# Performance work log

Hardware: AMD Instinct MI355X
Metric: run time of the kernel (lower is better)

## Reference

```python
import jax, jax.numpy as jnp
import numpy as np

B, N, E, D = 4, 50000, 800000, 64


def setup_inputs() -> dict:
    key = jax.random.key(0)
    k_h, k_e, k_w1, k_w2 = jax.random.split(key, 4)
    s = 1.0 / np.sqrt(D)  # glorot-ish scale for 64x64 linear weights
    return {
        "t": jnp.zeros((1,), jnp.float32),
        "h": jax.random.normal(k_h, (B, N, D), jnp.float32),
        "edge_index": jax.random.randint(k_e, (2, E), 0, N, jnp.int32),
        "W1": jax.random.normal(k_w1, (D, D), jnp.float32) * s,
        "b1": jnp.zeros((D,), jnp.float32),
        "W2": jax.random.normal(k_w2, (D, D), jnp.float32) * s,
        "b2": jnp.zeros((D,), jnp.float32),
    }


def _gcn(x, row, col, norm, W, b, n_nodes):
    # x: (B, N, D). PyG GCNConv: linear (no bias) -> normalized gather/scatter -> +bias
    xw = jnp.einsum("bnd,de->bne", x, W)
    msg = xw[:, row, :] * norm[None, :, None]          # (B, E+N, D)
    agg = jax.vmap(lambda m: jax.ops.segment_sum(m, col, num_segments=n_nodes))(msg)
    return agg + b


def reference(t, h, edge_index, W1, b1, W2, b2):
    n_nodes = h.shape[1]
    loop = jnp.arange(n_nodes, dtype=edge_index.dtype)
    # add self-loops (PyG GCNConv default)
    row = jnp.concatenate([edge_index[0], loop])  # source nodes
    col = jnp.concatenate([edge_index[1], loop])  # target nodes
    # symmetric normalization D^{-1/2} (A+I) D^{-1/2}; degree counted on targets
    deg = jax.ops.segment_sum(jnp.ones_like(row, dtype=h.dtype), col, num_segments=n_nodes)
    dis = jnp.where(deg > 0, jax.lax.rsqrt(deg), 0.0)
    norm = dis[row] * dis[col]
    h = jnp.tanh(_gcn(h, row, col, norm, W1, b1, n_nodes))
    h = jnp.tanh(_gcn(h, row, col, norm, W2, b2, n_nodes))
    return h
```

## Files before the change

### kernel.cpp

```cpp
#include <hip/hip_runtime.h>
#include <math.h>

#define B_ 4
#define N_ 50000
#define E_ 800000
#define D_ 64
#define M_ (B_*N_)
#define STRIDE_ 48

#define FILL_BLKS_ ((E_/4+255)/256)

typedef _Float16 h4 __attribute__((ext_vector_type(4)));
typedef _Float16 h8 __attribute__((ext_vector_type(8)));
typedef float    f4 __attribute__((ext_vector_type(4)));

__device__ __forceinline__ void wfrag_one(const float* __restrict__ W, h8* __restrict__ Wf, int fid) {
  int khalf = fid >> 8, rem = fid & 255, tt = rem >> 6, lane = rem & 63;
  int kq = lane >> 4, m = lane & 15;
  h8 v;
#pragma unroll
  for (int j = 0; j < 8; j++) {
    int k = khalf * 32 + kq * 8 + j;
    v[j] = (_Float16)W[k * 64 + tt * 16 + m];
  }
  Wf[fid] = v;
}

__global__ __launch_bounds__(256) void k_fill(const int4* __restrict__ row4, const int4* __restrict__ col4,
                                              int* __restrict__ cur, int* __restrict__ em,
                                              const float* __restrict__ W1, const float* __restrict__ W2,
                                              h8* __restrict__ Wf1, h8* __restrict__ Wf2) {
  if (blockIdx.x >= FILL_BLKS_) {
    int fa = (blockIdx.x - FILL_BLKS_) * 256 + threadIdx.x;
    if (fa < 512) wfrag_one(W1, Wf1, fa);
    else          wfrag_one(W2, Wf2, fa - 512);
    return;
  }
  int e = blockIdx.x * 256 + threadIdx.x;
  if (e < E_ / 4) {
    int4 c = col4[e];
    int4 r = row4[e];
    int k;
    k = atomicAdd(&cur[c.x], 1); if (k < STRIDE_) em[c.x * STRIDE_ + k] = r.x << 9;
    k = atomicAdd(&cur[c.y], 1); if (k < STRIDE_) em[c.y * STRIDE_ + k] = r.y << 9;
    k = atomicAdd(&cur[c.z], 1); if (k < STRIDE_) em[c.z * STRIDE_ + k] = r.z << 9;
    k = atomicAdd(&cur[c.w], 1); if (k < STRIDE_) em[c.w * STRIDE_ + k] = r.w << 9;
  }
}

template<int IN_F16>
__global__ __launch_bounds__(256) void k_linear(const void* __restrict__ Xv,
                                                const h8* __restrict__ Wf,
                                                const int* __restrict__ cur,
                                                _Float16* __restrict__ Y) {
  int wv = blockIdx.x * 4 + (threadIdx.x >> 6);
  int lane = threadIdx.x & 63;
  int m = lane & 15, kq = lane >> 4;
  size_t r0 = (size_t)wv * 16;
  h8 a0, a1;
  if constexpr (IN_F16) {
    const _Float16* xr = (const _Float16*)Xv + (r0 + m) * 64 + kq * 8;
    a0 = *(const h8*)(xr);
    a1 = *(const h8*)(xr + 32);
  } else {
    const float* xr = (const float*)Xv + (r0 + m) * 64 + kq * 8;
    f4 f0 = *(const f4*)(xr);
    f4 f1 = *(const f4*)(xr + 4);
    f4 f2 = *(const f4*)(xr + 32);
    f4 f3 = *(const f4*)(xr + 36);
#pragma unroll
    for (int j = 0; j < 4; j++) {
      a0[j] = (_Float16)f0[j]; a0[j + 4] = (_Float16)f1[j];
      a1[j] = (_Float16)f2[j]; a1[j + 4] = (_Float16)f3[j];
    }
  }
  f4 acc[4];
#pragma unroll
  for (int t = 0; t < 4; t++) {
    h8 b0 = Wf[t * 64 + lane];
    h8 b1 = Wf[256 + t * 64 + lane];
    f4 c = {0.f, 0.f, 0.f, 0.f};
    c = __builtin_amdgcn_mfma_f32_16x16x32_f16(a0, b0, c, 0, 0, 0);
    c = __builtin_amdgcn_mfma_f32_16x16x32_f16(a1, b1, c, 0, 0, 0);
    acc[t] = c;
  }
  int b  = (int)(r0 / N_);
  int n0 = (int)(r0 - (size_t)b * N_);
  float dv[4];
#pragma unroll
  for (int rr = 0; rr < 4; rr++) {
    int dg = cur[n0 + kq * 4 + rr];
    dv[rr] = 1.0f / sqrtf((float)(dg + 1));
  }
#pragma unroll
  for (int t = 0; t < 4; t++) {
#pragma unroll
    for (int rr = 0; rr < 4; rr++) {
      int n = n0 + kq * 4 + rr;
      Y[(size_t)n * 256 + b * 64 + t * 16 + m] = (_Float16)(acc[t][rr] * dv[rr]);
    }
  }
}

template<int OUT_F16>
__global__ __launch_bounds__(512) void k_agg(const _Float16* __restrict__ xw,
                                             const int* __restrict__ cur,
                                             const int* __restrict__ em,
                                             const float* __restrict__ bias,
                                             void* __restrict__ outv) {
  int node = blockIdx.x * 8 + (threadIdx.x >> 6);
  int lane = threadIdx.x & 63;
  const char* xb = (const char*)xw + (size_t)(lane * 8);
  int deg = __builtin_amdgcn_readfirstlane(cur[node]);
  if (deg > STRIDE_) deg = STRIDE_;
  float dc = 1.0f / sqrtf((float)(deg + 1));
  h4 sv = *(const h4*)(xb + ((size_t)node << 9));
  f4 acc = __builtin_convertvector(sv, f4);
  const int* eb = em + node * STRIDE_;
#define EDGE_(o) do { \
    h4 v_ = *(const h4*)(xb + (unsigned)(o)); \
    acc += __builtin_convertvector(v_, f4); \
  } while (0)
  int j = 0;
  for (; j + 8 <= deg; j += 8) {
    int o0 = eb[j],     o1 = eb[j + 1], o2 = eb[j + 2], o3 = eb[j + 3];
    int o4 = eb[j + 4], o5 = eb[j + 5], o6 = eb[j + 6], o7 = eb[j + 7];
    EDGE_(o0); EDGE_(o1); EDGE_(o2); EDGE_(o3);
    EDGE_(o4); EDGE_(o5); EDGE_(o6); EDGE_(o7);
  }
  for (; j < deg; ++j) { int o = eb[j]; EDGE_(o); }
#undef EDGE_
  int b  = lane >> 4;
  int d0 = (lane & 15) * 4;
  f4 bb = *(const f4*)(bias + d0);
  float r0 = tanhf(acc.x * dc + bb.x);
  float r1 = tanhf(acc.y * dc + bb.y);
  float r2 = tanhf(acc.z * dc + bb.z);
  float r3 = tanhf(acc.w * dc + bb.w);
  if constexpr (OUT_F16) {
    h4 o;
    o[0] = (_Float16)r0; o[1] = (_Float16)r1;
    o[2] = (_Float16)r2; o[3] = (_Float16)r3;
    *(h4*)((_Float16*)outv + ((size_t)b * N_ + node) * 64 + d0) = o;
  } else {
    f4 r = {r0, r1, r2, r3};
    *(f4*)((float*)outv + ((size_t)b * N_ + node) * 64 + d0) = r;
  }
}

extern "C" void kernel_launch(void* const* d_in, const int* in_sizes, int n_in,
                              void* d_out, int out_size, void* d_ws, size_t ws_size,
                              hipStream_t stream) {
  const float* h  = (const float*)d_in[1];
  const int*   ei = (const int*)d_in[2];
  const float* W1 = (const float*)d_in[3];
  const float* b1 = (const float*)d_in[4];
  const float* W2 = (const float*)d_in[5];
  const float* b2 = (const float*)d_in[6];
  float* out = (float*)d_out;
  const int* row = ei;
  const int* col = ei + E_;

  char* p = (char*)d_ws;
  _Float16* xw = (_Float16*)p; p += (size_t)M_ * D_ * sizeof(_Float16);
  int*  em  = (int*)p;    p += (size_t)N_ * STRIDE_ * sizeof(int);
  int*  cur = (int*)p;    p += (size_t)N_ * sizeof(int);
  h8*   Wf1 = (h8*)p;     p += 512 * sizeof(h8);
  h8*   Wf2 = (h8*)p;     p += 512 * sizeof(h8);
  _Float16* h1 = (_Float16*)d_out;

  hipMemsetAsync(cur, 0, N_ * sizeof(int), stream);

  k_fill<<<FILL_BLKS_ + 4, 256, 0, stream>>>((const int4*)row, (const int4*)col, cur, em, W1, W2, Wf1, Wf2);
  k_linear<0><<<M_ / 64, 256, 0, stream>>>(h, Wf1, cur, xw);
  k_agg<1><<<N_ / 8, 512, 0, stream>>>(xw, cur, em, b1, h1);
  k_linear<1><<<M_ / 64, 256, 0, stream>>>(h1, Wf2, cur, xw);
  k_agg<0><<<N_ / 8, 512, 0, stream>>>(xw, cur, em, b2, out);
}
```

Baseline: 298.3 us.

## Fuse second linear layer into first aggregation and pack edge indices to 16-bit

Performs the second layer's 64x64 linear transform inside the first aggregation kernel. It stages each node's tanh outputs in shared memory and runs MFMA, which removes one kernel launch and the intermediate write/read of the hidden activations. Edge source indices are stored as 16-bit values instead of pre-shifted 32-bit offsets, halving index storage and read traffic. The fused MFMA uses only 4 of 16 rows, wasting matrix throughput and adding a block barrier. The 16-bit indices rely on N fitting in 16 bits.

```diff
diff --git a/kernel.cpp b/kernel.cpp
--- a/kernel.cpp
+++ b/kernel.cpp
@@ -13,6 +13,8 @@
 typedef _Float16 h4 __attribute__((ext_vector_type(4)));
 typedef _Float16 h8 __attribute__((ext_vector_type(8)));
 typedef float    f4 __attribute__((ext_vector_type(4)));
+typedef unsigned short ushort_t;
+typedef unsigned int  uint_t;
 
 __device__ __forceinline__ void wfrag_one(const float* __restrict__ W, h8* __restrict__ Wf, int fid) {
   int khalf = fid >> 8, rem = fid & 255, tt = rem >> 6, lane = rem & 63;
@@ -27,7 +29,7 @@
 }
 
 __global__ __launch_bounds__(256) void k_fill(const int4* __restrict__ row4, const int4* __restrict__ col4,
-                                              int* __restrict__ cur, int* __restrict__ em,
+                                              int* __restrict__ cur, ushort_t* __restrict__ em,
                                               const float* __restrict__ W1, const float* __restrict__ W2,
                                               h8* __restrict__ Wf1, h8* __restrict__ Wf2) {
   if (blockIdx.x >= FILL_BLKS_) {
@@ -41,38 +43,31 @@
     int4 c = col4[e];
     int4 r = row4[e];
     int k;
-    k = atomicAdd(&cur[c.x], 1); if (k < STRIDE_) em[c.x * STRIDE_ + k] = r.x << 9;
-    k = atomicAdd(&cur[c.y], 1); if (k < STRIDE_) em[c.y * STRIDE_ + k] = r.y << 9;
-    k = atomicAdd(&cur[c.z], 1); if (k < STRIDE_) em[c.z * STRIDE_ + k] = r.z << 9;
-    k = atomicAdd(&cur[c.w], 1); if (k < STRIDE_) em[c.w * STRIDE_ + k] = r.w << 9;
-  }
-}
-
-template<int IN_F16>
-__global__ __launch_bounds__(256) void k_linear(const void* __restrict__ Xv,
-                                                const h8* __restrict__ Wf,
-                                                const int* __restrict__ cur,
-                                                _Float16* __restrict__ Y) {
+    k = atomicAdd(&cur[c.x], 1); if (k < STRIDE_) em[c.x * STRIDE_ + k] = (ushort_t)r.x;
+    k = atomicAdd(&cur[c.y], 1); if (k < STRIDE_) em[c.y * STRIDE_ + k] = (ushort_t)r.y;
+    k = atomicAdd(&cur[c.z], 1); if (k < STRIDE_) em[c.z * STRIDE_ + k] = (ushort_t)r.z;
+    k = atomicAdd(&cur[c.w], 1); if (k < STRIDE_) em[c.w * STRIDE_ + k] = (ushort_t)r.w;
+  }
+}
+
+__global__ __launch_bounds__(256) void k_linear1(const float* __restrict__ X,
+                                                 const h8* __restrict__ Wf,
+                                                 const int* __restrict__ cur,
+                                                 _Float16* __restrict__ Y) {
   int wv = blockIdx.x * 4 + (threadIdx.x >> 6);
   int lane = threadIdx.x & 63;
   int m = lane & 15, kq = lane >> 4;
   size_t r0 = (size_t)wv * 16;
+  const float* xr = X + (r0 + m) * 64 + kq * 8;
+  f4 f0 = *(const f4*)(xr);
+  f4 f1 = *(const f4*)(xr + 4);
+  f4 f2 = *(const f4*)(xr + 32);
+  f4 f3 = *(const f4*)(xr + 36);
   h8 a0, a1;
-  if constexpr (IN_F16) {
-    const _Float16* xr = (const _Float16*)Xv + (r0 + m) * 64 + kq * 8;
-    a0 = *(const h8*)(xr);
-    a1 = *(const h8*)(xr + 32);
-  } else {
-    const float* xr = (const float*)Xv + (r0 + m) * 64 + kq * 8;
-    f4 f0 = *(const f4*)(xr);
-    f4 f1 = *(const f4*)(xr + 4);
-    f4 f2 = *(const f4*)(xr + 32);
-    f4 f3 = *(const f4*)(xr + 36);
-#pragma unroll
-    for (int j = 0; j < 4; j++) {
-      a0[j] = (_Float16)f0[j]; a0[j + 4] = (_Float16)f1[j];
-      a1[j] = (_Float16)f2[j]; a1[j + 4] = (_Float16)f3[j];
-    }
+#pragma unroll
+  for (int j = 0; j < 4; j++) {
+    a0[j] = (_Float16)f0[j]; a0[j + 4] = (_Float16)f1[j];
+    a1[j] = (_Float16)f2[j]; a1[j + 4] = (_Float16)f3[j];
   }
   f4 acc[4];
 #pragma unroll
@@ -102,50 +97,111 @@
   }
 }
 
-template<int OUT_F16>
-__global__ __launch_bounds__(512) void k_agg(const _Float16* __restrict__ xw,
-                                             const int* __restrict__ cur,
-                                             const int* __restrict__ em,
-                                             const float* __restrict__ bias,
-                                             void* __restrict__ outv) {
+#define AGG_GATHER_(xb, eb, deg, acc)                                            \
+  do {                                                                           \
+    int j_ = 0;                                                                  \
+    for (; j_ + 8 <= (deg); j_ += 8) {                                           \
+      uint_t u0 = (eb)[(j_ >> 1)],     u1 = (eb)[(j_ >> 1) + 1];                 \
+      uint_t u2 = (eb)[(j_ >> 1) + 2], u3 = (eb)[(j_ >> 1) + 3];                 \
+      h4 v0 = *(const h4*)((xb) + ((u0 & 0xFFFFu) << 9));                        \
+      h4 v1 = *(const h4*)((xb) + ((u0 >> 16) << 9));                            \
+      h4 v2 = *(const h4*)((xb) + ((u1 & 0xFFFFu) << 9));                        \
+      h4 v3 = *(const h4*)((xb) + ((u1 >> 16) << 9));                            \
+      h4 v4 = *(const h4*)((xb) + ((u2 & 0xFFFFu) << 9));                        \
+      h4 v5 = *(const h4*)((xb) + ((u2 >> 16) << 9));                            \
+      h4 v6 = *(const h4*)((xb) + ((u3 & 0xFFFFu) << 9));                        \
+      h4 v7 = *(const h4*)((xb) + ((u3 >> 16) << 9));                            \
+      acc += __builtin_convertvector(v0, f4);                                    \
+      acc += __builtin_convertvector(v1, f4);                                    \
+      acc += __builtin_convertvector(v2, f4);                                    \
+      acc += __builtin_convertvector(v3, f4);                                    \
+      acc += __builtin_convertvector(v4, f4);                                    \
+      acc += __builtin_convertvector(v5, f4);                                    \
+      acc += __builtin_convertvector(v6, f4);                                    \
+      acc += __builtin_convertvector(v7, f4);                                    \
+    }                                                                            \
+    for (; j_ < (deg); ++j_) {                                                   \
+      uint_t u_ = (eb)[j_ >> 1];                                                 \
+      uint_t o_ = ((j_ & 1) ? (u_ >> 16) : (u_ & 0xFFFFu)) << 9;                 \
+      h4 v_ = *(const h4*)((xb) + o_);                                           \
+      acc += __builtin_convertvector(v_, f4);                                    \
+    }                                                                            \
+  } while (0)
+
+__global__ __launch_bounds__(512) void k_agg1(const _Float16* __restrict__ xw,
+                                              const int* __restrict__ cur,
+                                              const ushort_t* __restrict__ em,
+                                              const float* __restrict__ bias,
+                                              const h8* __restrict__ Wf,
+                                              _Float16* __restrict__ Y) {
+  __shared__ _Float16 ys[8][256];
+  int w    = threadIdx.x >> 6;
+  int node = blockIdx.x * 8 + w;
+  int lane = threadIdx.x & 63;
+  const char* xb = (const char*)xw + (size_t)(lane * 8);
+  int degt = __builtin_amdgcn_readfirstlane(cur[node]);
+  int deg  = degt > STRIDE_ ? STRIDE_ : degt;
+  float dc = 1.0f / sqrtf((float)(degt + 1));
+  h4 sv = *(const h4*)(xb + ((size_t)node << 9));
+  f4 acc = __builtin_convertvector(sv, f4);
+  const uint_t* eb = (const uint_t*)(em + node * STRIDE_);
+  AGG_GATHER_(xb, eb, deg, acc);
+  int d0 = (lane & 15) * 4;
+  f4 bb = *(const f4*)(bias + d0);
+  h4 yv;
+  yv[0] = (_Float16)tanhf(acc.x * dc + bb.x);
+  yv[1] = (_Float16)tanhf(acc.y * dc + bb.y);
+  yv[2] = (_Float16)tanhf(acc.z * dc + bb.z);
+  yv[3] = (_Float16)tanhf(acc.w * dc + bb.w);
+  *(h4*)&ys[w][lane * 4] = yv;
+  __syncthreads();
+  int m = lane & 15, kq = lane >> 4;
+  h8 a0, a1;
+#pragma unroll
+  for (int q = 0; q < 8; q++) { a0[q] = (_Float16)0.f; a1[q] = (_Float16)0.f; }
+  if (m < 4) {
+    a0 = *(const h8*)&ys[w][m * 64 + kq * 8];
+    a1 = *(const h8*)&ys[w][m * 64 + 32 + kq * 8];
+  }
+#pragma unroll
+  for (int t = 0; t < 4; t++) {
+    h8 b0 = Wf[t * 64 + lane];
+    h8 b1 = Wf[256 + t * 64 + lane];
+    f4 c = {0.f, 0.f, 0.f, 0.f};
+    c = __builtin_amdgcn_mfma_f32_16x16x32_f16(a0, b0, c, 0, 0, 0);
+    c = __builtin_amdgcn_mfma_f32_16x16x32_f16(a1, b1, c, 0, 0, 0);
+    if (kq == 0) {
+#pragma unroll
+      for (int b2 = 0; b2 < 4; b2++)
+        Y[(size_t)node * 256 + b2 * 64 + t * 16 + m] = (_Float16)(c[b2] * dc);
+    }
+  }
+}
+
+__global__ __launch_bounds__(512) void k_agg2(const _Float16* __restrict__ xw,
+                                              const int* __restrict__ cur,
+                                              const ushort_t* __restrict__ em,
+                                              const float* __restrict__ bias,
+                                              float* __restrict__ out) {
   int node = blockIdx.x * 8 + (threadIdx.x >> 6);
   int lane = threadIdx.x & 63;
   const char* xb = (const char*)xw + (size_t)(lane * 8);
-  int deg = __builtin_amdgcn_readfirstlane(cur[node]);
-  if (deg > STRIDE_) deg = STRIDE_;
-  float dc = 1.0f / sqrtf((float)(deg + 1));
+  int degt = __builtin_amdgcn_readfirstlane(cur[node]);
+  int deg  = degt > STRIDE_ ? STRIDE_ : degt;
+  float dc = 1.0f / sqrtf((float)(degt + 1));
   h4 sv = *(const h4*)(xb + ((size_t)node << 9));
   f4 acc = __builtin_convertvector(sv, f4);
-  const int* eb = em + node * STRIDE_;
-#define EDGE_(o) do { \
-    h4 v_ = *(const h4*)(xb + (unsigned)(o)); \
-    acc += __builtin_convertvector(v_, f4); \
-  } while (0)
-  int j = 0;
-  for (; j + 8 <= deg; j += 8) {
-    int o0 = eb[j],     o1 = eb[j + 1], o2 = eb[j + 2], o3 = eb[j + 3];
-    int o4 = eb[j + 4], o5 = eb[j + 5], o6 = eb[j + 6], o7 = eb[j + 7];
-    EDGE_(o0); EDGE_(o1); EDGE_(o2); EDGE_(o3);
-    EDGE_(o4); EDGE_(o5); EDGE_(o6); EDGE_(o7);
-  }
-  for (; j < deg; ++j) { int o = eb[j]; EDGE_(o); }
-#undef EDGE_
+  const uint_t* eb = (const uint_t*)(em + node * STRIDE_);
+  AGG_GATHER_(xb, eb, deg, acc);
   int b  = lane >> 4;
   int d0 = (lane & 15) * 4;
   f4 bb = *(const f4*)(bias + d0);
-  float r0 = tanhf(acc.x * dc + bb.x);
-  float r1 = tanhf(acc.y * dc + bb.y);
-  float r2 = tanhf(acc.z * dc + bb.z);
-  float r3 = tanhf(acc.w * dc + bb.w);
-  if constexpr (OUT_F16) {
-    h4 o;
-    o[0] = (_Float16)r0; o[1] = (_Float16)r1;
-    o[2] = (_Float16)r2; o[3] = (_Float16)r3;
-    *(h4*)((_Float16*)outv + ((size_t)b * N_ + node) * 64 + d0) = o;
-  } else {
-    f4 r = {r0, r1, r2, r3};
-    *(f4*)((float*)outv + ((size_t)b * N_ + node) * 64 + d0) = r;
-  }
+  f4 r;
+  r.x = tanhf(acc.x * dc + bb.x);
+  r.y = tanhf(acc.y * dc + bb.y);
+  r.z = tanhf(acc.z * dc + bb.z);
+  r.w = tanhf(acc.w * dc + bb.w);
+  *(f4*)(out + ((size_t)b * N_ + node) * 64 + d0) = r;
 }
 
 extern "C" void kernel_launch(void* const* d_in, const int* in_sizes, int n_in,
@@ -162,18 +218,17 @@
   const int* col = ei + E_;
 
   char* p = (char*)d_ws;
-  _Float16* xw = (_Float16*)p; p += (size_t)M_ * D_ * sizeof(_Float16);
-  int*  em  = (int*)p;    p += (size_t)N_ * STRIDE_ * sizeof(int);
+  _Float16* xw2 = (_Float16*)p; p += (size_t)M_ * D_ * sizeof(_Float16);
+  ushort_t* em  = (ushort_t*)p; p += (size_t)N_ * STRIDE_ * sizeof(ushort_t);
   int*  cur = (int*)p;    p += (size_t)N_ * sizeof(int);
   h8*   Wf1 = (h8*)p;     p += 512 * sizeof(h8);
   h8*   Wf2 = (h8*)p;     p += 512 * sizeof(h8);
-  _Float16* h1 = (_Float16*)d_out;
+  _Float16* xw1 = (_Float16*)d_out;
 
   hipMemsetAsync(cur, 0, N_ * sizeof(int), stream);
 
   k_fill<<<FILL_BLKS_ + 4, 256, 0, stream>>>((const int4*)row, (const int4*)col, cur, em, W1, W2, Wf1, Wf2);
-  k_linear<0><<<M_ / 64, 256, 0, stream>>>(h, Wf1, cur, xw);
-  k_agg<1><<<N_ / 8, 512, 0, stream>>>(xw, cur, em, b1, h1);
-  k_linear<1><<<M_ / 64, 256, 0, stream>>>(h1, Wf2, cur, xw);
-  k_agg<0><<<N_ / 8, 512, 0, stream>>>(xw, cur, em, b2, out);
-}
+  k_linear1<<<M_ / 64, 256, 0, stream>>>(h, Wf1, cur, xw1);
+  k_agg1<<<N_ / 8, 512, 0, stream>>>(xw1, cur, em, b1, Wf2, xw2);
+  k_agg2<<<N_ / 8, 512, 0, stream>>>(xw2, cur, em, b2, out);
+}
```

Measured after the change: 302.8 us. Within noise of the previous version (+1.5%).
